# Kernel optimization log

Hardware: AMD Instinct MI355X
Metric: run time of the kernel (lower is better)

The kernel has to match this reference:

```python
import jax, jax.numpy as jnp
import numpy as np

B, H, S, D = 2, 16, 2048, 128


def setup_inputs() -> dict:
    key = jax.random.key(0)
    kq, kk, kv, km = jax.random.split(key, 4)
    q = jax.random.normal(kq, (B, H, S, D), dtype=jnp.float32)
    k = jax.random.normal(kk, (B, H, S, D), dtype=jnp.float32)
    v = jax.random.normal(kv, (B, H, S, D), dtype=jnp.float32)
    mask = jax.random.randint(km, (1, 1, S, S), 0, 2, dtype=jnp.int32)
    return {"q": q, "k": k, "v": v, "mask": mask}


def reference(q, k, v, mask):
    b, h, s, d = v.shape
    # Faithful to the original: k.view(batch, n_head, d_tensor, seq_len) is a
    # RESHAPE (not a transpose) in the source, so we reshape here too.
    k_t = k.reshape(b, h, d, s)
    attn_score = jnp.matmul(q, k_t) / jnp.sqrt(jnp.float32(d))  # [B,H,S,S]
    # Original uses masked_fill(mask == 0, -e) with e=1e-12 (a tiny negative).
    score = jnp.where(mask == 0, jnp.float32(-1e-12), attn_score)
    # Original nn.Softmax() has no dim; PyTorch's legacy default for 4D input
    # is dim=1 (the head axis). Replicate that literally.
    score = jax.nn.softmax(score, axis=1)
    out = jnp.matmul(score, v)  # [B,H,S,D]
    return (out, score)
```

## Files before the change

### kernel.cpp

```cpp
#include <hip/hip_runtime.h>


#define SS 2048
#define DD 128
#define HH 16
#define BB 2

typedef short bf16x8 __attribute__((ext_vector_type(8)));
typedef float f32x4 __attribute__((ext_vector_type(4)));

__device__ __forceinline__ unsigned short f2bf(float f) {
  union { float f; unsigned u; } x; x.f = f;
  unsigned u = x.u;
  unsigned r = u + 0x7fffu + ((u >> 16) & 1u);
  return (unsigned short)(r >> 16);
}

__global__ __launch_bounds__(256)
void gemm_bf16(const float* __restrict__ Ag, const float* __restrict__ Bg,
               float* __restrict__ Cg, int Kdim,
               long lda, long ldb, long ldc,
               long sA, long sB, long sC, float scale)
{
  constexpr int BM = 128, BN = 128, BK = 64, LDSK = BK + 8;
  const float* A = Ag + (long)blockIdx.z * sA;
  const float* B = Bg + (long)blockIdx.z * sB;
  float*       C = Cg + (long)blockIdx.z * sC;
  const int i0 = blockIdx.x * BM;
  const int j0 = blockIdx.y * BN;
  const int tid  = threadIdx.x;
  const int lane = tid & 63;
  const int wv   = tid >> 6;
  const int wr   = (wv >> 1) * 64;
  const int wc   = (wv & 1) * 64;
  const int l15  = lane & 15;
  const int lhi  = lane >> 4;

  __shared__ unsigned short As[BM][LDSK];
  __shared__ unsigned short Bt[BN][LDSK];

  f32x4 acc[4][4];
  #pragma unroll
  for (int a = 0; a < 4; ++a)
    #pragma unroll
    for (int b = 0; b < 4; ++b)
      acc[a][b] = (f32x4){0.f, 0.f, 0.f, 0.f};

  for (int k0 = 0; k0 < Kdim; k0 += BK) {
    #pragma unroll
    for (int it = 0; it < 8; ++it) {
      const int lin = tid + it * 256;
      const int row = lin >> 4;
      const int c4  = lin & 15;
      const float4 v = *reinterpret_cast<const float4*>(
          A + (long)(i0 + row) * lda + (k0 + c4 * 4));
      ushort4 sv;
      sv.x = f2bf(v.x); sv.y = f2bf(v.y); sv.z = f2bf(v.z); sv.w = f2bf(v.w);
      *reinterpret_cast<ushort4*>(&As[row][c4 * 4]) = sv;
    }
    #pragma unroll
    for (int it = 0; it < 8; ++it) {
      const int lin = tid + it * 256;
      const int kr  = lin >> 5;
      const int j4  = lin & 31;
      const float4 v = *reinterpret_cast<const float4*>(
          B + (long)(k0 + kr) * ldb + (j0 + j4 * 4));
      Bt[j4 * 4 + 0][kr] = f2bf(v.x);
      Bt[j4 * 4 + 1][kr] = f2bf(v.y);
      Bt[j4 * 4 + 2][kr] = f2bf(v.z);
      Bt[j4 * 4 + 3][kr] = f2bf(v.w);
    }
    __syncthreads();
    #pragma unroll
    for (int kk = 0; kk < 2; ++kk) {
      const int kcol = kk * 32 + lhi * 8;
      bf16x8 afr[4], bfr[4];
      #pragma unroll
      for (int mi = 0; mi < 4; ++mi)
        afr[mi] = *reinterpret_cast<const bf16x8*>(&As[wr + mi * 16 + l15][kcol]);
      #pragma unroll
      for (int ni = 0; ni < 4; ++ni)
        bfr[ni] = *reinterpret_cast<const bf16x8*>(&Bt[wc + ni * 16 + l15][kcol]);
      #pragma unroll
      for (int mi = 0; mi < 4; ++mi)
        #pragma unroll
        for (int ni = 0; ni < 4; ++ni)
          acc[mi][ni] = __builtin_amdgcn_mfma_f32_16x16x32_bf16(
              afr[mi], bfr[ni], acc[mi][ni], 0, 0, 0);
    }
    __syncthreads();
  }

  #pragma unroll
  for (int mi = 0; mi < 4; ++mi) {
    #pragma unroll
    for (int ni = 0; ni < 4; ++ni) {
      const int col = j0 + wc + ni * 16 + l15;
      #pragma unroll
      for (int r = 0; r < 4; ++r) {
        const int row = i0 + wr + mi * 16 + lhi * 4 + r;
        C[(long)row * ldc + col] = acc[mi][ni][r] * scale;
      }
    }
  }
}

__global__ __launch_bounds__(256)
void softmax_heads(float* __restrict__ sc, const int* __restrict__ mask)
{
  const unsigned gid = blockIdx.x * 256u + threadIdx.x;
  const int j4 = gid & 511;
  const int i  = (gid >> 9) & 2047;
  const int b  = gid >> 20;
  const long PL = (long)SS * SS;
  const long off = (long)b * HH * PL + (long)i * SS + j4 * 4;

  const int4 mk = *reinterpret_cast<const int4*>(mask + (long)i * SS + j4 * 4);

  float4 s[16];
  #pragma unroll
  for (int h = 0; h < HH; ++h) {
    float4 v = *reinterpret_cast<const float4*>(sc + off + (long)h * PL);
    v.x = mk.x ? v.x : 0.0f;
    v.y = mk.y ? v.y : 0.0f;
    v.z = mk.z ? v.z : 0.0f;
    v.w = mk.w ? v.w : 0.0f;
    s[h] = v;
  }
  float4 mx = s[0];
  #pragma unroll
  for (int h = 1; h < HH; ++h) {
    mx.x = fmaxf(mx.x, s[h].x);
    mx.y = fmaxf(mx.y, s[h].y);
    mx.z = fmaxf(mx.z, s[h].z);
    mx.w = fmaxf(mx.w, s[h].w);
  }
  float4 sum = {0.f, 0.f, 0.f, 0.f};
  #pragma unroll
  for (int h = 0; h < HH; ++h) {
    s[h].x = __expf(s[h].x - mx.x);
    s[h].y = __expf(s[h].y - mx.y);
    s[h].z = __expf(s[h].z - mx.z);
    s[h].w = __expf(s[h].w - mx.w);
    sum.x += s[h].x; sum.y += s[h].y; sum.z += s[h].z; sum.w += s[h].w;
  }
  const float4 inv = {1.0f / sum.x, 1.0f / sum.y, 1.0f / sum.z, 1.0f / sum.w};
  #pragma unroll
  for (int h = 0; h < HH; ++h) {
    float4 o;
    o.x = s[h].x * inv.x; o.y = s[h].y * inv.y;
    o.z = s[h].z * inv.z; o.w = s[h].w * inv.w;
    *reinterpret_cast<float4*>(sc + off + (long)h * PL) = o;
  }
}

extern "C" void kernel_launch(void* const* d_in, const int* in_sizes, int n_in,
                              void* d_out, int out_size, void* d_ws, size_t ws_size,
                              hipStream_t stream)
{
  const float* q  = (const float*)d_in[0];
  const float* k  = (const float*)d_in[1];
  const float* v  = (const float*)d_in[2];
  const int* mask = (const int*)d_in[3];

  float* out   = (float*)d_out;
  float* score = out + (long)BB * HH * SS * DD;

  const long sQK = (long)SS * DD;
  const long sSC = (long)SS * SS;

  gemm_bf16<<<dim3(SS / 128, SS / 128, BB * HH), 256, 0, stream>>>(
      q, k, score, DD,
      (long)DD, (long)SS, (long)SS,
      sQK, sQK, sSC, 0.08838834764831845f);

  softmax_heads<<<dim3((BB * SS * (SS / 4)) / 256), 256, 0, stream>>>(score, mask);

  gemm_bf16<<<dim3(SS / 128, DD / 128, BB * HH), 256, 0, stream>>>(
      score, v, out, SS,
      (long)SS, (long)DD, (long)DD,
      sSC, sQK, sQK, 1.0f);
}
```

Before: 1.383 ms.

## Fuse QK^T GEMM with cross-head softmax into a single kernel

Replaces the separate QK^T GEMM and head-axis softmax kernels with one kernel. Each 32x32 output tile computes the scores for all 16 heads in registers, then applies the mask, scale and the softmax over heads before writing the final probabilities. This drops one full write and one read-modify-write pass over the large score tensor. The cost is small tiles with little operand reuse, repeated Q/K loads across tiles that depend on L2 hits, and transposed LDS stores for K that may cause bank conflicts.

```diff
diff --git a/kernel.cpp b/kernel.cpp
--- a/kernel.cpp
+++ b/kernel.cpp
@@ -14,6 +14,109 @@
   unsigned u = x.u;
   unsigned r = u + 0x7fffu + ((u >> 16) & 1u);
   return (unsigned short)(r >> 16);
+}
+
+__global__ __launch_bounds__(256)
+void qk_softmax_fused(const float* __restrict__ q, const float* __restrict__ k,
+                      const int* __restrict__ mask, float* __restrict__ score)
+{
+  constexpr int LK = DD + 8;
+  const int flat = blockIdx.x;
+  const int swz  = (flat & 7) * 1024 + (flat >> 3);
+  const int jt = swz & 63;
+  const int it = (swz >> 6) & 63;
+  const int b  = swz >> 12;
+  const int i0 = it * 32;
+  const int j0 = jt * 32;
+
+  const int tid  = threadIdx.x;
+  const int lane = tid & 63;
+  const int wv   = tid >> 6;
+  const int wi16 = (wv >> 1) * 16;
+  const int wj16 = (wv & 1) * 16;
+  const int l15  = lane & 15;
+  const int lhi  = lane >> 4;
+
+  const float* qb = q + (long)b * HH * SS * DD;
+  const float* kb = k + (long)b * HH * SS * DD;
+
+  __shared__ unsigned short As[2][32][LK];
+  __shared__ unsigned short Bk[2][32][LK];
+
+  f32x4 acc[HH];
+  #pragma unroll
+  for (int h = 0; h < HH; ++h) acc[h] = (f32x4){0.f, 0.f, 0.f, 0.f};
+
+  #pragma unroll
+  for (int hp = 0; hp < 8; ++hp) {
+    const int h0 = hp * 2;
+    #pragma unroll
+    for (int itr = 0; itr < 8; ++itr) {
+      const int idx = tid + itr * 256;
+      const int hh  = idx >> 10;
+      const int rem = idx & 1023;
+      const int row = rem >> 5;
+      const int c4  = rem & 31;
+      const float4 v = *reinterpret_cast<const float4*>(
+          qb + ((long)(h0 + hh) * SS + (i0 + row)) * DD + c4 * 4);
+      ushort4 sv;
+      sv.x = f2bf(v.x); sv.y = f2bf(v.y); sv.z = f2bf(v.z); sv.w = f2bf(v.w);
+      *reinterpret_cast<ushort4*>(&As[hh][row][c4 * 4]) = sv;
+    }
+    #pragma unroll
+    for (int itr = 0; itr < 8; ++itr) {
+      const int idx = tid + itr * 256;
+      const int hh  = idx >> 10;
+      const int rem = idx & 1023;
+      const int kr  = rem >> 3;
+      const int j4  = rem & 7;
+      const float4 v = *reinterpret_cast<const float4*>(
+          kb + (long)(h0 + hh) * SS * DD + (long)kr * SS + j0 + j4 * 4);
+      Bk[hh][j4 * 4 + 0][kr] = f2bf(v.x);
+      Bk[hh][j4 * 4 + 1][kr] = f2bf(v.y);
+      Bk[hh][j4 * 4 + 2][kr] = f2bf(v.z);
+      Bk[hh][j4 * 4 + 3][kr] = f2bf(v.w);
+    }
+    __syncthreads();
+    #pragma unroll
+    for (int hh = 0; hh < 2; ++hh) {
+      #pragma unroll
+      for (int kk = 0; kk < 4; ++kk) {
+        const int kcol = kk * 32 + lhi * 8;
+        const bf16x8 af = *reinterpret_cast<const bf16x8*>(&As[hh][wi16 + l15][kcol]);
+        const bf16x8 bf = *reinterpret_cast<const bf16x8*>(&Bk[hh][wj16 + l15][kcol]);
+        acc[h0 + hh] = __builtin_amdgcn_mfma_f32_16x16x32_bf16(af, bf, acc[h0 + hh], 0, 0, 0);
+      }
+    }
+    __syncthreads();
+  }
+
+  const float scale = 0.08838834764831845f;
+  const int col = j0 + wj16 + l15;
+  #pragma unroll
+  for (int r = 0; r < 4; ++r) {
+    const int row = i0 + wi16 + lhi * 4 + r;
+    const int m = mask[row * SS + col];
+    const float keep = m ? scale : 0.0f;
+    float sv[HH];
+    float mx = -1e30f;
+    #pragma unroll
+    for (int h = 0; h < HH; ++h) {
+      sv[h] = acc[h][r] * keep;
+      mx = fmaxf(mx, sv[h]);
+    }
+    float sum = 0.f;
+    #pragma unroll
+    for (int h = 0; h < HH; ++h) {
+      sv[h] = __expf(sv[h] - mx);
+      sum += sv[h];
+    }
+    const float inv = 1.0f / sum;
+    #pragma unroll
+    for (int h = 0; h < HH; ++h) {
+      score[(((long)b * HH + h) * SS + row) * SS + col] = sv[h] * inv;
+    }
+  }
 }
 
 __global__ __launch_bounds__(256)
@@ -43,13 +146,13 @@
   #pragma unroll
   for (int a = 0; a < 4; ++a)
     #pragma unroll
-    for (int b = 0; b < 4; ++b)
-      acc[a][b] = (f32x4){0.f, 0.f, 0.f, 0.f};
+    for (int b2 = 0; b2 < 4; ++b2)
+      acc[a][b2] = (f32x4){0.f, 0.f, 0.f, 0.f};
 
   for (int k0 = 0; k0 < Kdim; k0 += BK) {
     #pragma unroll
-    for (int it = 0; it < 8; ++it) {
-      const int lin = tid + it * 256;
+    for (int itr = 0; itr < 8; ++itr) {
+      const int lin = tid + itr * 256;
       const int row = lin >> 4;
       const int c4  = lin & 15;
       const float4 v = *reinterpret_cast<const float4*>(
@@ -59,8 +162,8 @@
       *reinterpret_cast<ushort4*>(&As[row][c4 * 4]) = sv;
     }
     #pragma unroll
-    for (int it = 0; it < 8; ++it) {
-      const int lin = tid + it * 256;
+    for (int itr = 0; itr < 8; ++itr) {
+      const int lin = tid + itr * 256;
       const int kr  = lin >> 5;
       const int j4  = lin & 31;
       const float4 v = *reinterpret_cast<const float4*>(
@@ -102,55 +205,6 @@
         C[(long)row * ldc + col] = acc[mi][ni][r] * scale;
       }
     }
-  }
-}
-
-__global__ __launch_bounds__(256)
-void softmax_heads(float* __restrict__ sc, const int* __restrict__ mask)
-{
-  const unsigned gid = blockIdx.x * 256u + threadIdx.x;
-  const int j4 = gid & 511;
-  const int i  = (gid >> 9) & 2047;
-  const int b  = gid >> 20;
-  const long PL = (long)SS * SS;
-  const long off = (long)b * HH * PL + (long)i * SS + j4 * 4;
-
-  const int4 mk = *reinterpret_cast<const int4*>(mask + (long)i * SS + j4 * 4);
-
-  float4 s[16];
-  #pragma unroll
-  for (int h = 0; h < HH; ++h) {
-    float4 v = *reinterpret_cast<const float4*>(sc + off + (long)h * PL);
-    v.x = mk.x ? v.x : 0.0f;
-    v.y = mk.y ? v.y : 0.0f;
-    v.z = mk.z ? v.z : 0.0f;
-    v.w = mk.w ? v.w : 0.0f;
-    s[h] = v;
-  }
-  float4 mx = s[0];
-  #pragma unroll
-  for (int h = 1; h < HH; ++h) {
-    mx.x = fmaxf(mx.x, s[h].x);
-    mx.y = fmaxf(mx.y, s[h].y);
-    mx.z = fmaxf(mx.z, s[h].z);
-    mx.w = fmaxf(mx.w, s[h].w);
-  }
-  float4 sum = {0.f, 0.f, 0.f, 0.f};
-  #pragma unroll
-  for (int h = 0; h < HH; ++h) {
-    s[h].x = __expf(s[h].x - mx.x);
-    s[h].y = __expf(s[h].y - mx.y);
-    s[h].z = __expf(s[h].z - mx.z);
-    s[h].w = __expf(s[h].w - mx.w);
-    sum.x += s[h].x; sum.y += s[h].y; sum.z += s[h].z; sum.w += s[h].w;
-  }
-  const float4 inv = {1.0f / sum.x, 1.0f / sum.y, 1.0f / sum.z, 1.0f / sum.w};
-  #pragma unroll
-  for (int h = 0; h < HH; ++h) {
-    float4 o;
-    o.x = s[h].x * inv.x; o.y = s[h].y * inv.y;
-    o.z = s[h].z * inv.z; o.w = s[h].w * inv.w;
-    *reinterpret_cast<float4*>(sc + off + (long)h * PL) = o;
   }
 }
 
@@ -169,12 +223,7 @@
   const long sQK = (long)SS * DD;
   const long sSC = (long)SS * SS;
 
-  gemm_bf16<<<dim3(SS / 128, SS / 128, BB * HH), 256, 0, stream>>>(
-      q, k, score, DD,
-      (long)DD, (long)SS, (long)SS,
-      sQK, sQK, sSC, 0.08838834764831845f);
-
-  softmax_heads<<<dim3((BB * SS * (SS / 4)) / 256), 256, 0, stream>>>(score, mask);
+  qk_softmax_fused<<<dim3(64 * 64 * BB), 256, 0, stream>>>(q, k, mask, score);
 
   gemm_bf16<<<dim3(SS / 128, DD / 128, BB * HH), 256, 0, stream>>>(
       score, v, out, SS,
```

New measurement: 1.418 ms. 2.5% more time.

## Store pre-softmax scores as bf16 in workspace and specialize the QK GEMM

Applied to the files above, without the earlier changes.

The QK^T GEMM now writes its scaled scores as bf16 into a workspace buffer instead of writing fp32 into the score output. The softmax reads that bf16 buffer, applies the mask by multiplication, and writes fp32 probabilities to the output. This halves the intermediate write and read traffic that previously went through the output in place. The dedicated QK kernel also fixes K=128 and reorganizes the K-tile loads into a vectorized 4x4 transpose for fewer LDS stores. The extra bf16 rounding of the scores adds precision loss, and the kernel relies on the workspace being large enough.

```diff
diff --git a/kernel.cpp b/kernel.cpp
--- a/kernel.cpp
+++ b/kernel.cpp
@@ -14,6 +14,160 @@
   unsigned u = x.u;
   unsigned r = u + 0x7fffu + ((u >> 16) & 1u);
   return (unsigned short)(r >> 16);
+}
+__device__ __forceinline__ float bf2f(unsigned short s) {
+  union { unsigned u; float f; } x; x.u = ((unsigned)s) << 16;
+  return x.f;
+}
+
+__global__ __launch_bounds__(256)
+void qk_gemm(const float* __restrict__ q, const float* __restrict__ k,
+             unsigned short* __restrict__ pre)
+{
+  constexpr int LDSK = 72;
+  const int z  = blockIdx.z;
+  const float* A = q + (long)z * SS * DD;
+  const float* B = k + (long)z * SS * DD;
+  unsigned short* C = pre + (long)z * SS * SS;
+  const int i0 = blockIdx.x * 128;
+  const int j0 = blockIdx.y * 128;
+  const int tid  = threadIdx.x;
+  const int lane = tid & 63;
+  const int wv   = tid >> 6;
+  const int wr   = (wv >> 1) * 64;
+  const int wc   = (wv & 1) * 64;
+  const int l15  = lane & 15;
+  const int lhi  = lane >> 4;
+
+  __shared__ unsigned short As[128][LDSK];
+  __shared__ unsigned short Bt[128][LDSK];
+
+  f32x4 acc[4][4];
+  #pragma unroll
+  for (int a = 0; a < 4; ++a)
+    #pragma unroll
+    for (int b2 = 0; b2 < 4; ++b2)
+      acc[a][b2] = (f32x4){0.f, 0.f, 0.f, 0.f};
+
+  #pragma unroll
+  for (int kp = 0; kp < 2; ++kp) {
+    const int k0 = kp * 64;
+    #pragma unroll
+    for (int it = 0; it < 8; ++it) {
+      const int lin = tid + it * 256;
+      const int row = lin >> 4;
+      const int c4  = lin & 15;
+      const float4 v = *reinterpret_cast<const float4*>(
+          A + (long)(i0 + row) * DD + (k0 + c4 * 4));
+      ushort4 sv;
+      sv.x = f2bf(v.x); sv.y = f2bf(v.y); sv.z = f2bf(v.z); sv.w = f2bf(v.w);
+      *reinterpret_cast<ushort4*>(&As[row][c4 * 4]) = sv;
+    }
+    #pragma unroll
+    for (int it = 0; it < 2; ++it) {
+      const int p    = tid + it * 256;
+      const int jgrp = (p & 7) + 8 * (p >> 7);
+      const int dgrp = (p >> 3) & 15;
+      float4 ld[4];
+      #pragma unroll
+      for (int c = 0; c < 4; ++c)
+        ld[c] = *reinterpret_cast<const float4*>(
+            B + (long)(k0 + dgrp * 4 + c) * SS + j0 + jgrp * 4);
+      #pragma unroll
+      for (int rr = 0; rr < 4; ++rr) {
+        ushort4 sv;
+        sv.x = f2bf(((const float*)&ld[0])[rr]);
+        sv.y = f2bf(((const float*)&ld[1])[rr]);
+        sv.z = f2bf(((const float*)&ld[2])[rr]);
+        sv.w = f2bf(((const float*)&ld[3])[rr]);
+        *reinterpret_cast<ushort4*>(&Bt[jgrp * 4 + rr][dgrp * 4]) = sv;
+      }
+    }
+    __syncthreads();
+    #pragma unroll
+    for (int kk = 0; kk < 2; ++kk) {
+      const int kcol = kk * 32 + lhi * 8;
+      bf16x8 afr[4], bfr[4];
+      #pragma unroll
+      for (int mi = 0; mi < 4; ++mi)
+        afr[mi] = *reinterpret_cast<const bf16x8*>(&As[wr + mi * 16 + l15][kcol]);
+      #pragma unroll
+      for (int ni = 0; ni < 4; ++ni)
+        bfr[ni] = *reinterpret_cast<const bf16x8*>(&Bt[wc + ni * 16 + l15][kcol]);
+      #pragma unroll
+      for (int mi = 0; mi < 4; ++mi)
+        #pragma unroll
+        for (int ni = 0; ni < 4; ++ni)
+          acc[mi][ni] = __builtin_amdgcn_mfma_f32_16x16x32_bf16(
+              afr[mi], bfr[ni], acc[mi][ni], 0, 0, 0);
+    }
+    __syncthreads();
+  }
+
+  const float scale = 0.08838834764831845f;
+  #pragma unroll
+  for (int mi = 0; mi < 4; ++mi) {
+    #pragma unroll
+    for (int ni = 0; ni < 4; ++ni) {
+      const int col = j0 + wc + ni * 16 + l15;
+      #pragma unroll
+      for (int r = 0; r < 4; ++r) {
+        const int row = i0 + wr + mi * 16 + lhi * 4 + r;
+        C[(long)row * SS + col] = f2bf(acc[mi][ni][r] * scale);
+      }
+    }
+  }
+}
+
+__global__ __launch_bounds__(256)
+void softmax_heads(const unsigned short* __restrict__ pre,
+                   const int* __restrict__ mask, float* __restrict__ score)
+{
+  const unsigned gid = blockIdx.x * 256u + threadIdx.x;
+  const int j4 = gid & 511;
+  const int i  = (gid >> 9) & 2047;
+  const int b  = gid >> 20;
+  const long PL = (long)SS * SS;
+  const long off = (long)b * HH * PL + (long)i * SS + j4 * 4;
+
+  const int4 mk = *reinterpret_cast<const int4*>(mask + (long)i * SS + j4 * 4);
+  const float k0 = mk.x ? 1.f : 0.f, k1 = mk.y ? 1.f : 0.f;
+  const float k2 = mk.z ? 1.f : 0.f, k3 = mk.w ? 1.f : 0.f;
+
+  float4 s[HH];
+  #pragma unroll
+  for (int h = 0; h < HH; ++h) {
+    const ushort4 u = *reinterpret_cast<const ushort4*>(pre + off + (long)h * PL);
+    s[h].x = bf2f(u.x) * k0;
+    s[h].y = bf2f(u.y) * k1;
+    s[h].z = bf2f(u.z) * k2;
+    s[h].w = bf2f(u.w) * k3;
+  }
+  float4 mx = s[0];
+  #pragma unroll
+  for (int h = 1; h < HH; ++h) {
+    mx.x = fmaxf(mx.x, s[h].x);
+    mx.y = fmaxf(mx.y, s[h].y);
+    mx.z = fmaxf(mx.z, s[h].z);
+    mx.w = fmaxf(mx.w, s[h].w);
+  }
+  float4 sum = {0.f, 0.f, 0.f, 0.f};
+  #pragma unroll
+  for (int h = 0; h < HH; ++h) {
+    s[h].x = __expf(s[h].x - mx.x);
+    s[h].y = __expf(s[h].y - mx.y);
+    s[h].z = __expf(s[h].z - mx.z);
+    s[h].w = __expf(s[h].w - mx.w);
+    sum.x += s[h].x; sum.y += s[h].y; sum.z += s[h].z; sum.w += s[h].w;
+  }
+  const float4 inv = {1.0f / sum.x, 1.0f / sum.y, 1.0f / sum.z, 1.0f / sum.w};
+  #pragma unroll
+  for (int h = 0; h < HH; ++h) {
+    float4 o;
+    o.x = s[h].x * inv.x; o.y = s[h].y * inv.y;
+    o.z = s[h].z * inv.z; o.w = s[h].w * inv.w;
+    *reinterpret_cast<float4*>(score + off + (long)h * PL) = o;
+  }
 }
 
 __global__ __launch_bounds__(256)
@@ -43,13 +197,13 @@
   #pragma unroll
   for (int a = 0; a < 4; ++a)
     #pragma unroll
-    for (int b = 0; b < 4; ++b)
-      acc[a][b] = (f32x4){0.f, 0.f, 0.f, 0.f};
+    for (int b2 = 0; b2 < 4; ++b2)
+      acc[a][b2] = (f32x4){0.f, 0.f, 0.f, 0.f};
 
   for (int k0 = 0; k0 < Kdim; k0 += BK) {
     #pragma unroll
-    for (int it = 0; it < 8; ++it) {
-      const int lin = tid + it * 256;
+    for (int itr = 0; itr < 8; ++itr) {
+      const int lin = tid + itr * 256;
       const int row = lin >> 4;
       const int c4  = lin & 15;
       const float4 v = *reinterpret_cast<const float4*>(
@@ -59,8 +213,8 @@
       *reinterpret_cast<ushort4*>(&As[row][c4 * 4]) = sv;
     }
     #pragma unroll
-    for (int it = 0; it < 8; ++it) {
-      const int lin = tid + it * 256;
+    for (int itr = 0; itr < 8; ++itr) {
+      const int lin = tid + itr * 256;
       const int kr  = lin >> 5;
       const int j4  = lin & 31;
       const float4 v = *reinterpret_cast<const float4*>(
@@ -105,55 +259,6 @@
   }
 }
 
-__global__ __launch_bounds__(256)
-void softmax_heads(float* __restrict__ sc, const int* __restrict__ mask)
-{
-  const unsigned gid = blockIdx.x * 256u + threadIdx.x;
-  const int j4 = gid & 511;
-  const int i  = (gid >> 9) & 2047;
-  const int b  = gid >> 20;
-  const long PL = (long)SS * SS;
-  const long off = (long)b * HH * PL + (long)i * SS + j4 * 4;
-
-  const int4 mk = *reinterpret_cast<const int4*>(mask + (long)i * SS + j4 * 4);
-
-  float4 s[16];
-  #pragma unroll
-  for (int h = 0; h < HH; ++h) {
-    float4 v = *reinterpret_cast<const float4*>(sc + off + (long)h * PL);
-    v.x = mk.x ? v.x : 0.0f;
-    v.y = mk.y ? v.y : 0.0f;
-    v.z = mk.z ? v.z : 0.0f;
-    v.w = mk.w ? v.w : 0.0f;
-    s[h] = v;
-  }
-  float4 mx = s[0];
-  #pragma unroll
-  for (int h = 1; h < HH; ++h) {
-    mx.x = fmaxf(mx.x, s[h].x);
-    mx.y = fmaxf(mx.y, s[h].y);
-    mx.z = fmaxf(mx.z, s[h].z);
-    mx.w = fmaxf(mx.w, s[h].w);
-  }
-  float4 sum = {0.f, 0.f, 0.f, 0.f};
-  #pragma unroll
-  for (int h = 0; h < HH; ++h) {
-    s[h].x = __expf(s[h].x - mx.x);
-    s[h].y = __expf(s[h].y - mx.y);
-    s[h].z = __expf(s[h].z - mx.z);
-    s[h].w = __expf(s[h].w - mx.w);
-    sum.x += s[h].x; sum.y += s[h].y; sum.z += s[h].z; sum.w += s[h].w;
-  }
-  const float4 inv = {1.0f / sum.x, 1.0f / sum.y, 1.0f / sum.z, 1.0f / sum.w};
-  #pragma unroll
-  for (int h = 0; h < HH; ++h) {
-    float4 o;
-    o.x = s[h].x * inv.x; o.y = s[h].y * inv.y;
-    o.z = s[h].z * inv.z; o.w = s[h].w * inv.w;
-    *reinterpret_cast<float4*>(sc + off + (long)h * PL) = o;
-  }
-}
-
 extern "C" void kernel_launch(void* const* d_in, const int* in_sizes, int n_in,
                               void* d_out, int out_size, void* d_ws, size_t ws_size,
                               hipStream_t stream)
@@ -165,16 +270,14 @@
 
   float* out   = (float*)d_out;
   float* score = out + (long)BB * HH * SS * DD;
+  unsigned short* pre = (unsigned short*)d_ws;
 
   const long sQK = (long)SS * DD;
   const long sSC = (long)SS * SS;
 
-  gemm_bf16<<<dim3(SS / 128, SS / 128, BB * HH), 256, 0, stream>>>(
-      q, k, score, DD,
-      (long)DD, (long)SS, (long)SS,
-      sQK, sQK, sSC, 0.08838834764831845f);
-
-  softmax_heads<<<dim3((BB * SS * (SS / 4)) / 256), 256, 0, stream>>>(score, mask);
+  qk_gemm<<<dim3(SS / 128, SS / 128, BB * HH), 256, 0, stream>>>(q, k, pre);
+
+  softmax_heads<<<dim3((BB * SS * (SS / 4)) / 256), 256, 0, stream>>>(pre, mask, score);
 
   gemm_bf16<<<dim3(SS / 128, DD / 128, BB * HH), 256, 0, stream>>>(
       score, v, out, SS,
```

Result: faster. 1.163 ms (-15.9%).
